# Performance work log

Hardware: AMD Instinct MI355X
Metric: run time of the kernel (lower is better)

The kernel has to match this reference:

```python
import jax, jax.numpy as jnp
import numpy as np

N_NODES = 100000
N_EDGES = 1600000
XN_DIM = 32
ATTR_DIM = 2 * 16 + 1  # xn_attr_dim*2 + 1 = 33


def tv_norm(x, eps=1e-3):
    x = x - jnp.mean(x, axis=1, keepdims=True)
    return x / jnp.sqrt(jnp.sum(x * x, axis=1, keepdims=True) + eps)


def setup_inputs() -> dict:
    key = jax.random.key(0)
    ks = jax.random.split(key, 7)
    xn = jax.random.normal(ks[0], (N_NODES, XN_DIM), dtype=jnp.float32)
    xe_attr = jax.random.normal(ks[1], (N_EDGES, ATTR_DIM), dtype=jnp.float32)
    # fc1: Linear(33 -> 32) with bias (stored as [in, out] for x @ W)
    W1 = jax.random.normal(ks[2], (ATTR_DIM, XN_DIM), dtype=jnp.float32) * (1.0 / np.sqrt(ATTR_DIM))
    b1 = jax.random.normal(ks[3], (XN_DIM,), dtype=jnp.float32) * 0.01
    # DoubleLayer lin1: Linear(5d -> 5d, bias=False); lin1 is applied TWICE in forward
    Wd1 = jax.random.normal(ks[4], (5 * XN_DIM, 5 * XN_DIM), dtype=jnp.float32) * (1.0 / np.sqrt(5 * XN_DIM))
    xe_src = jax.random.randint(ks[5], (N_EDGES,), 0, N_NODES, dtype=jnp.int64 if jax.config.jax_enable_x64 else jnp.int32)
    xe_dst = jax.random.randint(ks[6], (N_EDGES,), 0, N_NODES, dtype=jnp.int64 if jax.config.jax_enable_x64 else jnp.int32)
    return {"xn": xn, "xe_attr": xe_attr, "W1": W1, "b1": b1, "Wd1": Wd1,
            "xe_src": xe_src, "xe_dst": xe_dst}


def reference(xn, xe_attr, W1, b1, Wd1, xe_src, xe_dst):
    n, d = xn.shape
    # fc1: single Linear + silu activation at the end
    W = jax.nn.silu(xe_attr @ W1 + b1)               # [E, d]
    xs = xn[xe_src]                                   # gather [E, d]
    xd = xn[xe_dst]                                   # gather [E, d]
    gradX = W * (xs - xd)
    aveX = W * (xs + xd) * 0.5
    dxe = jnp.concatenate([gradX, aveX, gradX * aveX, gradX * gradX, aveX * aveX], axis=1)  # [E, 5d]
    # DoubleLayer: tanh -> lin1 -> tv_norm -> tanh -> lin1 -> tanh (lin1 used twice)
    x = jnp.tanh(dxe) @ Wd1
    x = tv_norm(x)
    x = jnp.tanh(x) @ Wd1
    dxe = jnp.tanh(x)
    msg = jnp.tile(W, (1, 5)) * dxe                   # W.repeat(1,5) * dxe
    xn_1 = jax.ops.segment_sum(msg, xe_dst, num_segments=n)  # scatter-add on dst
    xn_2 = jax.ops.segment_sum(msg, xe_src, num_segments=n)  # scatter-add on src
    xn_div = xn_1 - xn_2
    xn_ave = (xn_1 + xn_2) * 0.5
    out = (xn_div[:, :d] + xn_ave[:, d:2 * d] + xn_ave[:, 2 * d:3 * d]
           + xn_ave[:, 3 * d:4 * d] + xn_ave[:, 4 * d:])
    return out
```

## Files before the change

kernel.cpp:

```cpp
#include <hip/hip_runtime.h>
#include <cstdint>

constexpr int D      = 32;
constexpr int FD     = 160;
constexpr int ATTRD  = 33;
constexpr int WTILE  = 16;
constexpr int BLOCK  = 256;
constexpr int NKS    = 5;
constexpr int ASTR   = 168;
constexpr int SWSTR  = 36;
constexpr int WBYTES = 5376;

typedef __attribute__((ext_vector_type(8))) short short8;
typedef __attribute__((ext_vector_type(4))) float f32x4;

__device__ __forceinline__ float fast_tanh(float x) {
    float e = __expf(2.0f * x);
    return 1.0f - 2.0f * __builtin_amdgcn_rcpf(e + 1.0f);
}
__device__ __forceinline__ unsigned short bf16rne(float x) {
    union { float f; unsigned u; } v; v.f = x;
    unsigned r = v.u + 0x7fffu + ((v.u >> 16) & 1u);
    return (unsigned short)(r >> 16);
}

__global__ void prep_weights(const float* __restrict__ Wd1,
                             const float* __restrict__ W1,
                             unsigned short* __restrict__ wsb) {
    int t = blockIdx.x * blockDim.x + threadIdx.x;
    if (t < FD * FD) {
        int k = t / FD, n = t - k * FD;
        int nt = n >> 4, l15 = n & 15;
        int ks = k >> 5, quad = (k >> 3) & 3, j = k & 7;
        int dst = ((nt * NKS + ks) * 64 + quad * 16 + l15) * 8 + j;
        wsb[dst] = bf16rne(Wd1[t]);
    } else if (t < FD * FD + 32 * D) {
        int t2 = t - FD * FD;
        int k = t2 >> 5, n = t2 & 31;
        int nt = n >> 4, l15 = n & 15;
        int quad = k >> 3, j = k & 7;
        int dst = FD * FD + (nt * 64 + quad * 16 + l15) * 8 + j;
        wsb[dst] = bf16rne(W1[k * D + n]);
    }
}

__global__ __launch_bounds__(BLOCK, 5)
void prop_mfma(const float* __restrict__ xn,
               const float* __restrict__ xe_attr,
               const float* __restrict__ W1,
               const float* __restrict__ b1,
               const unsigned short* __restrict__ wsb,
               const int*   __restrict__ esrc,
               const int*   __restrict__ edst,
               float* __restrict__ out,
               int E)
{
    __shared__ __align__(16) unsigned char sMem[4 * WBYTES];

    const int tid  = threadIdx.x;
    const int lane = tid & 63;
    const int w    = tid >> 6;
    const int l15  = lane & 15;
    const int quad = lane >> 4;
    unsigned char* wbase = sMem + w * WBYTES;
    float*          sW = reinterpret_cast<float*>(wbase);
    unsigned short* sA = reinterpret_cast<unsigned short*>(wbase);

    const long tile = (long)blockIdx.x * 4 + w;
    const long e0   = tile * WTILE;
    if (e0 >= (long)E) return;
    const int nv = min(WTILE, (int)((long)E - e0));

    const short8* Bp  = reinterpret_cast<const short8*>(wsb);
    const short8* W1p = reinterpret_cast<const short8*>(wsb + FD * FD);

    float Wr0[4], Wr1[4];
    {
        int rowA = (int)e0 + ((l15 < nv) ? l15 : 0);
        const float* ar = xe_attr + (size_t)rowA * ATTRD + quad * 8;
        union { short8 v; unsigned short u[8]; } AF0;
        #pragma unroll
        for (int j = 0; j < 8; ++j) AF0.u[j] = bf16rne(ar[j]);

        f32x4 c0 = (f32x4){0.f, 0.f, 0.f, 0.f};
        f32x4 c1 = (f32x4){0.f, 0.f, 0.f, 0.f};
        c0 = __builtin_amdgcn_mfma_f32_16x16x32_bf16(AF0.v, W1p[lane],      c0, 0, 0, 0);
        c1 = __builtin_amdgcn_mfma_f32_16x16x32_bf16(AF0.v, W1p[64 + lane], c1, 0, 0, 0);

        float b1a  = b1[l15],            b1b  = b1[16 + l15];
        float w32a = W1[32 * D + l15],   w32b = W1[32 * D + 16 + l15];
        #pragma unroll
        for (int r = 0; r < 4; ++r) {
            int e = quad * 4 + r;
            int rowC = (int)e0 + ((e < nv) ? e : 0);
            float a32 = xe_attr[(size_t)rowC * ATTRD + 32];
            float x0 = c0[r] + b1a + a32 * w32a;
            float x1 = c1[r] + b1b + a32 * w32b;
            float s0 = x0 * __builtin_amdgcn_rcpf(1.0f + __expf(-x0));
            float s1 = x1 * __builtin_amdgcn_rcpf(1.0f + __expf(-x1));
            Wr0[r] = s0;
            Wr1[r] = s1;
            sW[e * SWSTR + l15]      = s0;
            sW[e * SWSTR + 16 + l15] = s1;
        }
    }

    {
        int ei = (int)e0 + ((l15 < nv) ? l15 : 0);
        int se = esrc[ei], de = edst[ei];
        const float4* xsr = reinterpret_cast<const float4*>(xn + (size_t)se * D + quad * 8);
        const float4* xdr = reinterpret_cast<const float4*>(xn + (size_t)de * D + quad * 8);
        float4 xs0 = xsr[0], xs1 = xsr[1];
        float4 xd0 = xdr[0], xd1 = xdr[1];
        float4 wv0 = *reinterpret_cast<const float4*>(&sW[l15 * SWSTR + quad * 8]);
        float4 wv1 = *reinterpret_cast<const float4*>(&sW[l15 * SWSTR + quad * 8 + 4]);
        float xs[8] = {xs0.x, xs0.y, xs0.z, xs0.w, xs1.x, xs1.y, xs1.z, xs1.w};
        float xd[8] = {xd0.x, xd0.y, xd0.z, xd0.w, xd1.x, xd1.y, xd1.z, xd1.w};
        float wf[8] = {wv0.x, wv0.y, wv0.z, wv0.w, wv1.x, wv1.y, wv1.z, wv1.w};
        union { short8 v; unsigned short u[8]; } T[5];
        #pragma unroll
        for (int c = 0; c < 8; ++c) {
            float g = wf[c] * (xs[c] - xd[c]);
            float a = wf[c] * (xs[c] + xd[c]) * 0.5f;
            T[0].u[c] = bf16rne(fast_tanh(g));
            T[1].u[c] = bf16rne(fast_tanh(a));
            T[2].u[c] = bf16rne(fast_tanh(g * a));
            T[3].u[c] = bf16rne(fast_tanh(g * g));
            T[4].u[c] = bf16rne(fast_tanh(a * a));
        }
        #pragma unroll
        for (int f = 0; f < 5; ++f)
            *reinterpret_cast<short8*>(&sA[l15 * ASTR + f * 32 + quad * 8]) = T[f].v;
    }

    f32x4 C[10];
    #pragma unroll
    for (int t = 0; t < 10; ++t) C[t] = (f32x4){0.f, 0.f, 0.f, 0.f};
    #pragma unroll
    for (int ks = 0; ks < NKS; ++ks) {
        short8 af1 = *reinterpret_cast<const short8*>(&sA[l15 * ASTR + ks * 32 + quad * 8]);
        #pragma unroll
        for (int nt = 0; nt < 10; ++nt)
            C[nt] = __builtin_amdgcn_mfma_f32_16x16x32_bf16(
                af1, Bp[(nt * NKS + ks) * 64 + lane], C[nt], 0, 0, 0);
    }

    float mean[4], scale[4];
    #pragma unroll
    for (int r = 0; r < 4; ++r) {
        float s = 0.f, q = 0.f;
        #pragma unroll
        for (int t = 0; t < 10; ++t) { float v = C[t][r]; s += v; q += v * v; }
        #pragma unroll
        for (int m = 1; m < 16; m <<= 1) { s += __shfl_xor(s, m); q += __shfl_xor(q, m); }
        mean[r] = s * (1.0f / FD);
        scale[r] = __builtin_amdgcn_rsqf(q - (float)FD * mean[r] * mean[r] + 1e-3f);
    }

    #pragma unroll
    for (int t = 0; t < 10; ++t)
        #pragma unroll
        for (int r = 0; r < 4; ++r) {
            float v = fast_tanh((C[t][r] - mean[r]) * scale[r]);
            sA[(quad * 4 + r) * ASTR + t * 16 + l15] = bf16rne(v);
        }

    #pragma unroll
    for (int t = 0; t < 10; ++t) C[t] = (f32x4){0.f, 0.f, 0.f, 0.f};
    #pragma unroll
    for (int ks = 0; ks < NKS; ++ks) {
        short8 af2 = *reinterpret_cast<const short8*>(&sA[l15 * ASTR + ks * 32 + quad * 8]);
        #pragma unroll
        for (int nt = 0; nt < 10; ++nt)
            C[nt] = __builtin_amdgcn_mfma_f32_16x16x32_bf16(
                af2, Bp[(nt * NKS + ks) * 64 + lane], C[nt], 0, 0, 0);
    }

    #pragma unroll
    for (int r = 0; r < 4; ++r) {
        int e = quad * 4 + r;
        if (e >= nv) continue;
        int sd = edst[e0 + e], ss = esrc[e0 + e];
        #pragma unroll
        for (int par = 0; par < 2; ++par) {
            int c = par * 16 + l15;
            float wv = (par == 0) ? Wr0[r] : Wr1[r];
            float m0 = fast_tanh(C[par][r]) * wv;
            float A4 = (fast_tanh(C[par + 2][r]) + fast_tanh(C[par + 4][r])
                      + fast_tanh(C[par + 6][r]) + fast_tanh(C[par + 8][r])) * wv;
            atomicAdd(out + (size_t)sd * D + c, m0 + 0.5f * A4);
            atomicAdd(out + (size_t)ss * D + c, 0.5f * A4 - m0);
        }
    }
}

extern "C" void kernel_launch(void* const* d_in, const int* in_sizes, int n_in,
                              void* d_out, int out_size, void* d_ws, size_t ws_size,
                              hipStream_t stream)
{
    const float* xn   = (const float*)d_in[0];
    const float* attr = (const float*)d_in[1];
    const float* W1   = (const float*)d_in[2];
    const float* b1   = (const float*)d_in[3];
    const float* Wd1  = (const float*)d_in[4];
    const int*   esrc = (const int*)d_in[5];
    const int*   edst = (const int*)d_in[6];
    float* out = (float*)d_out;
    unsigned short* wsb = (unsigned short*)d_ws;

    const int E = in_sizes[5];

    hipMemsetAsync(d_out, 0, (size_t)out_size * sizeof(float), stream);
    prep_weights<<<(FD * FD + 32 * D + 255) / 256, 256, 0, stream>>>(Wd1, W1, wsb);
    const long tiles = ((long)E + WTILE - 1) / WTILE;
    const int grid = (int)((tiles + 3) / 4);
    prop_mfma<<<grid, BLOCK, 0, stream>>>(xn, attr, W1, b1, wsb, esrc, edst, out, E);
}
```

Baseline: 918.2 us.

## Switch edge MLP to 32x32x16 MFMA with 32-edge wave tiles

Each wavefront now handles 32 edges instead of 16 and uses 32x32x16 bf16 MFMA instructions in place of 16x16x32. The prep kernel reorders the packed weight layout to match, and all fragment index maps, LDS staging and the row-wise tv_norm reductions are rewritten for the 32-row layout. The aim is fewer MFMA issues and weight-fragment reloads per edge, since each B fragment is reused across twice as many rows. In exchange the accumulator register footprint and LDS per wave roughly double, and launch bounds drop from 5 to 3 waves-per-SIMD, which lowers occupancy for this gather/atomic-heavy kernel.

```diff
diff --git a/kernel.cpp b/kernel.cpp
--- a/kernel.cpp
+++ b/kernel.cpp
@@ -4,15 +4,16 @@
 constexpr int D      = 32;
 constexpr int FD     = 160;
 constexpr int ATTRD  = 33;
-constexpr int WTILE  = 16;
+constexpr int WTILE  = 32;
 constexpr int BLOCK  = 256;
-constexpr int NKS    = 5;
+constexpr int NKS    = 10;
+constexpr int NNT    = 5;
 constexpr int ASTR   = 168;
 constexpr int SWSTR  = 36;
-constexpr int WBYTES = 5376;
-
-typedef __attribute__((ext_vector_type(8))) short short8;
-typedef __attribute__((ext_vector_type(4))) float f32x4;
+constexpr int WBYTES = 10752;
+
+typedef __attribute__((ext_vector_type(8)))  short short8;
+typedef __attribute__((ext_vector_type(16))) float f32x16;
 
 __device__ __forceinline__ float fast_tanh(float x) {
     float e = __expf(2.0f * x);
@@ -22,6 +23,9 @@
     union { float f; unsigned u; } v; v.f = x;
     unsigned r = v.u + 0x7fffu + ((v.u >> 16) & 1u);
     return (unsigned short)(r >> 16);
+}
+__device__ __forceinline__ f32x16 zero16() {
+    return (f32x16){0.f,0.f,0.f,0.f,0.f,0.f,0.f,0.f,0.f,0.f,0.f,0.f,0.f,0.f,0.f,0.f};
 }
 
 __global__ void prep_weights(const float* __restrict__ Wd1,
@@ -30,21 +34,20 @@
     int t = blockIdx.x * blockDim.x + threadIdx.x;
     if (t < FD * FD) {
         int k = t / FD, n = t - k * FD;
-        int nt = n >> 4, l15 = n & 15;
-        int ks = k >> 5, quad = (k >> 3) & 3, j = k & 7;
-        int dst = ((nt * NKS + ks) * 64 + quad * 16 + l15) * 8 + j;
+        int ks = k >> 4, half = (k >> 3) & 1, j = k & 7;
+        int nt = n >> 5, col = n & 31;
+        int dst = ((nt * NKS + ks) * 64 + half * 32 + col) * 8 + j;
         wsb[dst] = bf16rne(Wd1[t]);
     } else if (t < FD * FD + 32 * D) {
         int t2 = t - FD * FD;
         int k = t2 >> 5, n = t2 & 31;
-        int nt = n >> 4, l15 = n & 15;
-        int quad = k >> 3, j = k & 7;
-        int dst = FD * FD + (nt * 64 + quad * 16 + l15) * 8 + j;
+        int ks = k >> 4, half = (k >> 3) & 1, j = k & 7;
+        int dst = FD * FD + (ks * 64 + half * 32 + n) * 8 + j;
         wsb[dst] = bf16rne(W1[k * D + n]);
     }
 }
 
-__global__ __launch_bounds__(BLOCK, 5)
+__global__ __launch_bounds__(BLOCK, 3)
 void prop_mfma(const float* __restrict__ xn,
                const float* __restrict__ xe_attr,
                const float* __restrict__ W1,
@@ -60,8 +63,8 @@
     const int tid  = threadIdx.x;
     const int lane = tid & 63;
     const int w    = tid >> 6;
-    const int l15  = lane & 15;
-    const int quad = lane >> 4;
+    const int col  = lane & 31;
+    const int half = lane >> 5;
     unsigned char* wbase = sMem + w * WBYTES;
     float*          sW = reinterpret_cast<float*>(wbase);
     unsigned short* sA = reinterpret_cast<unsigned short*>(wbase);
@@ -74,123 +77,124 @@
     const short8* Bp  = reinterpret_cast<const short8*>(wsb);
     const short8* W1p = reinterpret_cast<const short8*>(wsb + FD * FD);
 
-    float Wr0[4], Wr1[4];
+    f32x16 Wc;
     {
-        int rowA = (int)e0 + ((l15 < nv) ? l15 : 0);
-        const float* ar = xe_attr + (size_t)rowA * ATTRD + quad * 8;
-        union { short8 v; unsigned short u[8]; } AF0;
-        #pragma unroll
-        for (int j = 0; j < 8; ++j) AF0.u[j] = bf16rne(ar[j]);
-
-        f32x4 c0 = (f32x4){0.f, 0.f, 0.f, 0.f};
-        f32x4 c1 = (f32x4){0.f, 0.f, 0.f, 0.f};
-        c0 = __builtin_amdgcn_mfma_f32_16x16x32_bf16(AF0.v, W1p[lane],      c0, 0, 0, 0);
-        c1 = __builtin_amdgcn_mfma_f32_16x16x32_bf16(AF0.v, W1p[64 + lane], c1, 0, 0, 0);
-
-        float b1a  = b1[l15],            b1b  = b1[16 + l15];
-        float w32a = W1[32 * D + l15],   w32b = W1[32 * D + 16 + l15];
-        #pragma unroll
-        for (int r = 0; r < 4; ++r) {
-            int e = quad * 4 + r;
-            int rowC = (int)e0 + ((e < nv) ? e : 0);
+        int rowA = (int)e0 + ((col < nv) ? col : 0);
+        const float* ar = xe_attr + (size_t)rowA * ATTRD;
+        union { short8 v; unsigned short u[8]; } A0, A1;
+        #pragma unroll
+        for (int j = 0; j < 8; ++j) {
+            A0.u[j] = bf16rne(ar[half * 8 + j]);
+            A1.u[j] = bf16rne(ar[16 + half * 8 + j]);
+        }
+        f32x16 c = zero16();
+        c = __builtin_amdgcn_mfma_f32_32x32x16_bf16(A0.v, W1p[lane],      c, 0, 0, 0);
+        c = __builtin_amdgcn_mfma_f32_32x32x16_bf16(A1.v, W1p[64 + lane], c, 0, 0, 0);
+
+        float b1c  = b1[col];
+        float w32c = W1[32 * D + col];
+        #pragma unroll
+        for (int r = 0; r < 16; ++r) {
+            int row  = (r & 3) + 8 * (r >> 2) + 4 * half;
+            int rowC = (int)e0 + ((row < nv) ? row : 0);
             float a32 = xe_attr[(size_t)rowC * ATTRD + 32];
-            float x0 = c0[r] + b1a + a32 * w32a;
-            float x1 = c1[r] + b1b + a32 * w32b;
-            float s0 = x0 * __builtin_amdgcn_rcpf(1.0f + __expf(-x0));
-            float s1 = x1 * __builtin_amdgcn_rcpf(1.0f + __expf(-x1));
-            Wr0[r] = s0;
-            Wr1[r] = s1;
-            sW[e * SWSTR + l15]      = s0;
-            sW[e * SWSTR + 16 + l15] = s1;
+            float x = c[r] + b1c + a32 * w32c;
+            float s = x * __builtin_amdgcn_rcpf(1.0f + __expf(-x));
+            Wc[r] = s;
+            sW[row * SWSTR + col] = s;
         }
     }
 
     {
-        int ei = (int)e0 + ((l15 < nv) ? l15 : 0);
+        int e  = (col < nv) ? col : 0;
+        int ei = (int)e0 + e;
         int se = esrc[ei], de = edst[ei];
-        const float4* xsr = reinterpret_cast<const float4*>(xn + (size_t)se * D + quad * 8);
-        const float4* xdr = reinterpret_cast<const float4*>(xn + (size_t)de * D + quad * 8);
-        float4 xs0 = xsr[0], xs1 = xsr[1];
-        float4 xd0 = xdr[0], xd1 = xdr[1];
-        float4 wv0 = *reinterpret_cast<const float4*>(&sW[l15 * SWSTR + quad * 8]);
-        float4 wv1 = *reinterpret_cast<const float4*>(&sW[l15 * SWSTR + quad * 8 + 4]);
-        float xs[8] = {xs0.x, xs0.y, xs0.z, xs0.w, xs1.x, xs1.y, xs1.z, xs1.w};
-        float xd[8] = {xd0.x, xd0.y, xd0.z, xd0.w, xd1.x, xd1.y, xd1.z, xd1.w};
-        float wf[8] = {wv0.x, wv0.y, wv0.z, wv0.w, wv1.x, wv1.y, wv1.z, wv1.w};
-        union { short8 v; unsigned short u[8]; } T[5];
-        #pragma unroll
-        for (int c = 0; c < 8; ++c) {
-            float g = wf[c] * (xs[c] - xd[c]);
-            float a = wf[c] * (xs[c] + xd[c]) * 0.5f;
-            T[0].u[c] = bf16rne(fast_tanh(g));
-            T[1].u[c] = bf16rne(fast_tanh(a));
-            T[2].u[c] = bf16rne(fast_tanh(g * a));
-            T[3].u[c] = bf16rne(fast_tanh(g * g));
-            T[4].u[c] = bf16rne(fast_tanh(a * a));
-        }
-        #pragma unroll
-        for (int f = 0; f < 5; ++f)
-            *reinterpret_cast<short8*>(&sA[l15 * ASTR + f * 32 + quad * 8]) = T[f].v;
-    }
-
-    f32x4 C[10];
-    #pragma unroll
-    for (int t = 0; t < 10; ++t) C[t] = (f32x4){0.f, 0.f, 0.f, 0.f};
+        const float* xsp = xn + (size_t)se * D;
+        const float* xdp = xn + (size_t)de * D;
+        float4 wfa = *reinterpret_cast<const float4*>(&sW[e * SWSTR + half * 8]);
+        float4 wfb = *reinterpret_cast<const float4*>(&sW[e * SWSTR + half * 8 + 4]);
+        float4 wfc = *reinterpret_cast<const float4*>(&sW[e * SWSTR + 16 + half * 8]);
+        float4 wfd = *reinterpret_cast<const float4*>(&sW[e * SWSTR + 16 + half * 8 + 4]);
+        float wf16[16] = {wfa.x,wfa.y,wfa.z,wfa.w, wfb.x,wfb.y,wfb.z,wfb.w,
+                          wfc.x,wfc.y,wfc.z,wfc.w, wfd.x,wfd.y,wfd.z,wfd.w};
+        #pragma unroll
+        for (int p = 0; p < 2; ++p) {
+            int cb = p * 16 + half * 8;
+            float4 xsa = *reinterpret_cast<const float4*>(xsp + cb);
+            float4 xsb = *reinterpret_cast<const float4*>(xsp + cb + 4);
+            float4 xda = *reinterpret_cast<const float4*>(xdp + cb);
+            float4 xdb = *reinterpret_cast<const float4*>(xdp + cb + 4);
+            float xs8[8] = {xsa.x,xsa.y,xsa.z,xsa.w, xsb.x,xsb.y,xsb.z,xsb.w};
+            float xd8[8] = {xda.x,xda.y,xda.z,xda.w, xdb.x,xdb.y,xdb.z,xdb.w};
+            union { short8 v; unsigned short u[8]; } T[5];
+            #pragma unroll
+            for (int c = 0; c < 8; ++c) {
+                float wfv = wf16[p * 8 + c];
+                float g = wfv * (xs8[c] - xd8[c]);
+                float a = wfv * (xs8[c] + xd8[c]) * 0.5f;
+                T[0].u[c] = bf16rne(fast_tanh(g));
+                T[1].u[c] = bf16rne(fast_tanh(a));
+                T[2].u[c] = bf16rne(fast_tanh(g * a));
+                T[3].u[c] = bf16rne(fast_tanh(g * g));
+                T[4].u[c] = bf16rne(fast_tanh(a * a));
+            }
+            #pragma unroll
+            for (int f = 0; f < 5; ++f)
+                *reinterpret_cast<short8*>(&sA[e * ASTR + f * 32 + cb]) = T[f].v;
+        }
+    }
+
+    f32x16 C[NNT];
+    #pragma unroll
+    for (int t = 0; t < NNT; ++t) C[t] = zero16();
     #pragma unroll
     for (int ks = 0; ks < NKS; ++ks) {
-        short8 af1 = *reinterpret_cast<const short8*>(&sA[l15 * ASTR + ks * 32 + quad * 8]);
-        #pragma unroll
-        for (int nt = 0; nt < 10; ++nt)
-            C[nt] = __builtin_amdgcn_mfma_f32_16x16x32_bf16(
-                af1, Bp[(nt * NKS + ks) * 64 + lane], C[nt], 0, 0, 0);
-    }
-
-    float mean[4], scale[4];
-    #pragma unroll
-    for (int r = 0; r < 4; ++r) {
+        short8 af = *reinterpret_cast<const short8*>(&sA[col * ASTR + ks * 16 + half * 8]);
+        #pragma unroll
+        for (int nt = 0; nt < NNT; ++nt)
+            C[nt] = __builtin_amdgcn_mfma_f32_32x32x16_bf16(
+                af, Bp[(nt * NKS + ks) * 64 + lane], C[nt], 0, 0, 0);
+    }
+
+    #pragma unroll
+    for (int r = 0; r < 16; ++r) {
         float s = 0.f, q = 0.f;
         #pragma unroll
-        for (int t = 0; t < 10; ++t) { float v = C[t][r]; s += v; q += v * v; }
-        #pragma unroll
-        for (int m = 1; m < 16; m <<= 1) { s += __shfl_xor(s, m); q += __shfl_xor(q, m); }
-        mean[r] = s * (1.0f / FD);
-        scale[r] = __builtin_amdgcn_rsqf(q - (float)FD * mean[r] * mean[r] + 1e-3f);
-    }
-
-    #pragma unroll
-    for (int t = 0; t < 10; ++t)
-        #pragma unroll
-        for (int r = 0; r < 4; ++r) {
-            float v = fast_tanh((C[t][r] - mean[r]) * scale[r]);
-            sA[(quad * 4 + r) * ASTR + t * 16 + l15] = bf16rne(v);
-        }
-
-    #pragma unroll
-    for (int t = 0; t < 10; ++t) C[t] = (f32x4){0.f, 0.f, 0.f, 0.f};
+        for (int nt = 0; nt < NNT; ++nt) { float v = C[nt][r]; s += v; q += v * v; }
+        #pragma unroll
+        for (int m = 1; m < 32; m <<= 1) { s += __shfl_xor(s, m); q += __shfl_xor(q, m); }
+        float mean = s * (1.0f / FD);
+        float sc = __builtin_amdgcn_rsqf(q - (float)FD * mean * mean + 1e-3f);
+        int row = (r & 3) + 8 * (r >> 2) + 4 * half;
+        #pragma unroll
+        for (int nt = 0; nt < NNT; ++nt) {
+            float v = fast_tanh((C[nt][r] - mean) * sc);
+            sA[row * ASTR + nt * 32 + col] = bf16rne(v);
+        }
+    }
+
+    #pragma unroll
+    for (int t = 0; t < NNT; ++t) C[t] = zero16();
     #pragma unroll
     for (int ks = 0; ks < NKS; ++ks) {
-        short8 af2 = *reinterpret_cast<const short8*>(&sA[l15 * ASTR + ks * 32 + quad * 8]);
-        #pragma unroll
-        for (int nt = 0; nt < 10; ++nt)
-            C[nt] = __builtin_amdgcn_mfma_f32_16x16x32_bf16(
-                af2, Bp[(nt * NKS + ks) * 64 + lane], C[nt], 0, 0, 0);
-    }
-
-    #pragma unroll
-    for (int r = 0; r < 4; ++r) {
-        int e = quad * 4 + r;
-        if (e >= nv) continue;
-        int sd = edst[e0 + e], ss = esrc[e0 + e];
-        #pragma unroll
-        for (int par = 0; par < 2; ++par) {
-            int c = par * 16 + l15;
-            float wv = (par == 0) ? Wr0[r] : Wr1[r];
-            float m0 = fast_tanh(C[par][r]) * wv;
-            float A4 = (fast_tanh(C[par + 2][r]) + fast_tanh(C[par + 4][r])
-                      + fast_tanh(C[par + 6][r]) + fast_tanh(C[par + 8][r])) * wv;
-            atomicAdd(out + (size_t)sd * D + c, m0 + 0.5f * A4);
-            atomicAdd(out + (size_t)ss * D + c, 0.5f * A4 - m0);
-        }
+        short8 af = *reinterpret_cast<const short8*>(&sA[col * ASTR + ks * 16 + half * 8]);
+        #pragma unroll
+        for (int nt = 0; nt < NNT; ++nt)
+            C[nt] = __builtin_amdgcn_mfma_f32_32x32x16_bf16(
+                af, Bp[(nt * NKS + ks) * 64 + lane], C[nt], 0, 0, 0);
+    }
+
+    #pragma unroll
+    for (int r = 0; r < 16; ++r) {
+        int row = (r & 3) + 8 * (r >> 2) + 4 * half;
+        if (row >= nv) continue;
+        int sd = edst[e0 + row], ss = esrc[e0 + row];
+        float wv = Wc[r];
+        float m0 = fast_tanh(C[0][r]) * wv;
+        float A4 = (fast_tanh(C[1][r]) + fast_tanh(C[2][r])
+                  + fast_tanh(C[3][r]) + fast_tanh(C[4][r])) * wv;
+        atomicAdd(out + (size_t)sd * D + col, m0 + 0.5f * A4);
+        atomicAdd(out + (size_t)ss * D + col, 0.5f * A4 - m0);
     }
 }
 
```

Measured after the change: 774.3 us. -15.7%, faster.
